# Kernel optimization log

Measured on AMD Instinct MI355X. Metric: run time of the kernel, lower is better.

## Reference

```python
import jax, jax.numpy as jnp
import numpy as np

NUM_COMPONENTS = 8
STRIDE, PADDING, OUTPUT_PADDING, K = 2, 1, 0, 4


def get_comp_mat(n):
    # Cayley-Dickson construction: entry [i, j] = +/- component index of the
    # weight multiplying input component j to produce output component i.
    A = np.array([[0]])
    while A.shape[0] < n:
        m = A.shape[0]
        A = np.vstack([np.hstack([A, -(A + m)]), np.hstack([A + m, A])])
    return A


def setup_inputs() -> dict:
    key = jax.random.key(0)
    k1, k2, k3 = jax.random.split(key, 3)
    B, Cin, Cout, H = 8, 512, 256, 64
    c_in, c_out = Cin // NUM_COMPONENTS, Cout // NUM_COMPONENTS
    x = jax.random.normal(k1, (B, Cin, H, H), jnp.float32)
    # per-component ConvTranspose2d weights, torch layout [C_in, C_out, kH, kW]
    W = jax.random.normal(k2, (NUM_COMPONENTS, c_in, c_out, K, K), jnp.float32) * 0.05
    b = jax.random.normal(k3, (NUM_COMPONENTS, c_out), jnp.float32) * 0.05
    return {"x": x, "W": W, "b": b}


def reference(x, W, b):
    n = NUM_COMPONENTS
    comp = get_comp_mat(n)                 # static [n, n] signed component table
    signs = jnp.asarray(np.where(comp < 0, -1.0, 1.0), x.dtype)
    idx = np.abs(comp)                     # which sub-conv weight to use
    c_in, c_out, kh, kw = W.shape[1:]
    # Fuse the n^2 transpose convs into ONE block transpose conv:
    # Kbig[j*c_in:(j+1)*c_in, i*c_out:(i+1)*c_out] = sign[i,j] * W[idx[i,j]]
    Wsel = W[idx] * signs[:, :, None, None, None, None]          # [ni, nj, c_in, c_out, kh, kw]
    Wbig = jnp.transpose(Wsel, (1, 2, 0, 3, 4, 5)).reshape(n * c_in, n * c_out, kh, kw)
    bbig = jnp.einsum('ij,ijc->ic', signs, b[idx]).reshape(n * c_out)
    # torch ConvTranspose2d == conv with input dilated by stride and flipped kernel
    rhs = jnp.flip(Wbig, (2, 3)).transpose(1, 0, 2, 3)           # OIHW
    pad = K - 1 - PADDING
    out = jax.lax.conv_general_dilated(
        x, rhs, window_strides=(1, 1),
        padding=((pad, pad + OUTPUT_PADDING), (pad, pad + OUTPUT_PADDING)),
        lhs_dilation=(STRIDE, STRIDE),
        dimension_numbers=('NCHW', 'OIHW', 'NCHW'))
    return out + bbig[None, :, None, None]
```

## Files before the change

kernel.cpp:

```cpp
#include <hip/hip_runtime.h>
#include <hip/hip_bf16.h>

typedef unsigned short ushort_t;
typedef __attribute__((ext_vector_type(8))) short short8;
typedef __attribute__((ext_vector_type(4))) float f32x4;

#define NCOMP    8
#define CIN      512
#define COUT     256
#define H        64
#define HP       66
#define OHW      128
#define NB       8

__device__ const int d_idx8[8][8] = {
    {0,1,2,1,4,3,2,3},
    {1,0,3,2,5,4,1,2},
    {2,1,0,1,6,5,4,3},
    {3,2,1,0,7,6,5,4},
    {4,3,2,3,0,1,2,1},
    {5,4,1,2,1,0,3,2},
    {6,5,4,3,2,1,0,1},
    {7,6,5,4,3,2,1,0}};

__device__ const int kh_tab[2][2] = {{1,3},{0,2}};
__device__ const int dh_tab[2][2] = {{0,-1},{1,0}};

__global__ void prep_x2(const float* __restrict__ x, ushort_t* __restrict__ xpadT) {
    __shared__ __align__(16) ushort_t lds[64 * 512];
    const int t = threadIdx.x;
    const int b = blockIdx.y;
    const int ihb = blockIdx.x;

    if (ihb == 64) {
        short8 z = {0,0,0,0,0,0,0,0};
        ushort_t* r0 = xpadT + ((size_t)b * HP + 0)  * HP * CIN;
        ushort_t* r1 = xpadT + ((size_t)b * HP + 65) * HP * CIN;
        for (int e = t; e < (HP * CIN) / 8; e += 256) {
            *(short8*)(r0 + e * 8) = z;
            *(short8*)(r1 + e * 8) = z;
        }
        return;
    }
    const int ih = ihb;

    const int iv      = t & 15;
    const int ic_base = t >> 4;
    const float* xr = x + ((size_t)b * CIN * H + ih) * H;
#pragma unroll 8
    for (int r = 0; r < 32; ++r) {
        const int ic = r * 16 + ic_base;
        const float4 v = *(const float4*)(xr + (size_t)ic * H * H + iv * 4);
        const int swz_ic = ic ^ (iv << 3);
        __hip_bfloat16 h0 = __float2bfloat16(v.x);
        __hip_bfloat16 h1 = __float2bfloat16(v.y);
        __hip_bfloat16 h2 = __float2bfloat16(v.z);
        __hip_bfloat16 h3 = __float2bfloat16(v.w);
        lds[(iv * 4 + 0) * 512 + swz_ic] = *(ushort_t*)&h0;
        lds[(iv * 4 + 1) * 512 + swz_ic] = *(ushort_t*)&h1;
        lds[(iv * 4 + 2) * 512 + swz_ic] = *(ushort_t*)&h2;
        lds[(iv * 4 + 3) * 512 + swz_ic] = *(ushort_t*)&h3;
    }
    __syncthreads();

    ushort_t* rowc = xpadT + (((size_t)b * HP + ih + 1) * HP) * CIN;
    ushort_t* dst  = rowc + CIN;
#pragma unroll
    for (int r = 0; r < 16; ++r) {
        const int e   = r * 256 + t;
        const int iw  = e >> 6;
        const int ic0 = (e & 63) * 8;
        const int off = iw * 512 + (ic0 ^ ((iw >> 2) << 3));
        *(short8*)(dst + (size_t)e * 8) = *(const short8*)(lds + off);
    }
    if (t < 128) {
        short8 z = {0,0,0,0,0,0,0,0};
        const int l = t & 63;
        ushort_t* hc = (t < 64) ? rowc : (rowc + 65 * CIN);
        *(short8*)(hc + l * 8) = z;
    }
}

__global__ void prep_w(const float* __restrict__ W, const float* __restrict__ bias,
                       ushort_t* __restrict__ Abf, float* __restrict__ bbig) {
    const int t = blockIdx.x * blockDim.x + threadIdx.x;
    if (t < 4 * 64 * 256 * 32) {
        int kin = t & 31;
        int oc  = (t >> 5) & 255;
        int ks  = (t >> 13) & 63;
        int cls = t >> 19;
        int k  = ks * 32 + kin;
        int a  = k >> 10, c = (k >> 9) & 1, ic = k & 511;
        int ph = cls >> 1, pw = cls & 1;
        int kh = kh_tab[ph][a], kw = kh_tab[pw][c];
        int i = oc >> 5, co = oc & 31;
        int j = ic >> 6, ci = ic & 63;
        float s = (i >= j) ? 1.0f : -1.0f;
        float v = s * W[(((size_t)(d_idx8[i][j] * 64 + ci) * 32 + co) * 4 + kh) * 4 + kw];
        __hip_bfloat16 h = __float2bfloat16(v);
        Abf[t] = *(ushort_t*)&h;
    }
    if (t < COUT) {
        int i = t >> 5, co = t & 31;
        float acc = 0.0f;
        for (int j = 0; j < NCOMP; ++j)
            acc += ((i >= j) ? 1.0f : -1.0f) * bias[d_idx8[i][j] * 32 + co];
        bbig[t] = acc;
    }
}

__device__ __forceinline__ void async16(void* lds_dst, const void* g_src) {
    __builtin_amdgcn_global_load_lds(
        (const __attribute__((address_space(1))) unsigned int*)g_src,
        (__attribute__((address_space(3))) unsigned int*)lds_dst,
        16, 0, 0);
}

#define STAGE(NS, CB)                                                          \
  {                                                                            \
    const int ns_  = (NS);                                                     \
    const int na_  = ns_ >> 5;                                                 \
    const int ncb_ = (ns_ >> 4) & 1;                                           \
    const int go_  = ((na_ ? dh1 : dh0) * HP + (ncb_ ? dw1 : dw0)) * CIN       \
                     + (ns_ & 15) * 32;                                        \
    const ushort_t* nap_ = Abf_t + (size_t)ns_ * 8192;                         \
    async16(sb + (CB) + t * 16,         nap_);                                 \
    async16(sb + (CB) + 8192 + t * 16,  base_lo + go_);                        \
    async16(sb + (CB) + 16384 + t * 16, base_hi + go_);                        \
  }

#define COMPUTE(CB)                                                            \
  {                                                                            \
    short8 af[4], bf[4];                                                       \
    _Pragma("unroll")                                                          \
    for (int s = 0; s < 4; ++s) {                                              \
      af[s] = *(const short8*)(sb + (CB) + aoff + s * 1024);                   \
      bf[s] = *(const short8*)(sb + (CB) + boff + s * 1024);                   \
    }                                                                          \
    _Pragma("unroll")                                                          \
    for (int sm = 0; sm < 4; ++sm)                                             \
      _Pragma("unroll")                                                        \
      for (int sn = 0; sn < 4; ++sn)                                           \
        acc[sm][sn] = __builtin_amdgcn_mfma_f32_16x16x32_bf16(                 \
            af[sm], bf[sn], acc[sm][sn], 0, 0, 0);                             \
  }

#define WAITBAR(N)                                                             \
  asm volatile("s_waitcnt vmcnt(" #N ")" ::: "memory");                        \
  __builtin_amdgcn_s_barrier();                                                \
  __builtin_amdgcn_sched_barrier(0);

__launch_bounds__(512, 4)
__global__ void htconv_mfma(const ushort_t* __restrict__ xpadT,
                            const ushort_t* __restrict__ Abf,
                            const float* __restrict__ bbig,
                            float* __restrict__ out) {
    __shared__ __align__(16) ushort_t smem[36864];
    char* sb = (char*)smem;

    const int t     = threadIdx.x;
    const int ntile = blockIdx.x;
    const int mtile = blockIdx.y;
    const int cls   = blockIdx.z & 3;
    const int b     = blockIdx.z >> 2;
    const int ph = cls >> 1, pw = cls & 1;
    const int ohh0 = ntile * 4;

    const int srcc = (((t & 3) ^ ((t >> 3) & 3)) * 8);
    const ushort_t* Abf_t =
        Abf + ((size_t)cls * 64) * 8192 + (size_t)mtile * 4096
            + ((size_t)(t >> 2)) * 32 + srcc;

    const int dh0 = dh_tab[ph][0], dh1 = dh_tab[ph][1];
    const int dw0 = dh_tab[pw][0], dw1 = dh_tab[pw][1];
    const int oww = (t >> 2) & 63;
    const int rlo = t >> 8;
    const ushort_t* base_lo =
        xpadT + (((size_t)b * HP + ohh0 + rlo + 1) * HP + oww + 1) * CIN + srcc;
    const ushort_t* base_hi = base_lo + (size_t)2 * HP * CIN;

    const int lane = t & 63, wave = t >> 6;
    const int wm = wave >> 2, wn = wave & 3;
    const int col = lane & 15, quad = lane >> 4;
    const int soff = (quad ^ ((col >> 1) & 3)) * 16;
    const int aoff = (wm * 64 + col) * 64 + soff;
    const int boff = 8192 + (wn * 64 + col) * 64 + soff;

    f32x4 acc[4][4];
#pragma unroll
    for (int i = 0; i < 4; ++i)
#pragma unroll
        for (int j = 0; j < 4; ++j)
            acc[i][j] = (f32x4){0.f, 0.f, 0.f, 0.f};

    STAGE(0, 0);
    STAGE(1, 24576);

#pragma unroll 1
    for (int i = 0; i < 20; ++i) {
        const int n = 3 * i;
        WAITBAR(3); STAGE(n + 2, 49152); COMPUTE(0);
        WAITBAR(3); STAGE(n + 3, 0);     COMPUTE(24576);
        WAITBAR(3); STAGE(n + 4, 24576); COMPUTE(49152);
    }
    WAITBAR(3); STAGE(62, 49152); COMPUTE(0);
    WAITBAR(3); STAGE(63, 0);     COMPUTE(24576);
    WAITBAR(3);                   COMPUTE(49152);
    WAITBAR(0);                   COMPUTE(0);

    const int oh = 2 * (ohh0 + wn) + ph;
#pragma unroll
    for (int sm = 0; sm < 4; ++sm) {
#pragma unroll
        for (int r = 0; r < 4; ++r) {
            const int occ = mtile * 128 + wm * 64 + sm * 16 + quad * 4 + r;
            const float bv = bbig[occ];
            float* obase = out + (((size_t)b * COUT + occ) * OHW + oh) * OHW + pw;
#pragma unroll
            for (int sn = 0; sn < 4; ++sn) {
                const int owi = sn * 16 + col;
                obase[2 * owi] = acc[sm][sn][r] + bv;
            }
        }
    }
}

extern "C" void kernel_launch(void* const* d_in, const int* in_sizes, int n_in,
                              void* d_out, int out_size, void* d_ws, size_t ws_size,
                              hipStream_t stream) {
    const float* x    = (const float*)d_in[0];
    const float* W    = (const float*)d_in[1];
    const float* bias = (const float*)d_in[2];
    float* out = (float*)d_out;

    ushort_t* xpadT = (ushort_t*)d_ws;
    ushort_t* Abf   = xpadT + (size_t)NB * HP * HP * CIN;
    float*    bbig  = (float*)(Abf + (size_t)4 * 64 * 256 * 32);

    prep_x2<<<dim3(65, NB), 256, 0, stream>>>(x, xpadT);
    prep_w<<<dim3((4 * 64 * 256 * 32) / 256), 256, 0, stream>>>(W, bias, Abf, bbig);
    htconv_mfma<<<dim3(16, 2, 32), 512, 0, stream>>>(xpadT, Abf, bbig, out);
}
```

Before: 310.9 us.

## Double-buffer LDS fragment reads in registers to overlap with MFMA

The main loop now software-pipelines the LDS-to-register fragment loads. Each step reads the next stage's A/B fragments into a second register set while issuing MFMAs on the current set, and the loop is unrolled by six to rotate both buffers. The wait before each barrier tightens from vmcnt(3) to vmcnt(0), so each step waits for the async copy issued one step earlier, with less slack for global-load latency. The extra fragment registers may also pressure occupancy under launch_bounds(512,4).

```diff
diff --git a/kernel.cpp b/kernel.cpp
--- a/kernel.cpp
+++ b/kernel.cpp
@@ -129,26 +129,29 @@
     async16(sb + (CB) + 16384 + t * 16, base_hi + go_);                        \
   }
 
-#define COMPUTE(CB)                                                            \
-  {                                                                            \
-    short8 af[4], bf[4];                                                       \
+#define DSREAD(CB, AFS, BFS)                                                   \
     _Pragma("unroll")                                                          \
     for (int s = 0; s < 4; ++s) {                                              \
-      af[s] = *(const short8*)(sb + (CB) + aoff + s * 1024);                   \
-      bf[s] = *(const short8*)(sb + (CB) + boff + s * 1024);                   \
-    }                                                                          \
+      AFS[s] = *(const short8*)(sb + (CB) + aoff + s * 1024);                  \
+      BFS[s] = *(const short8*)(sb + (CB) + boff + s * 1024);                  \
+    }
+
+#define MFMA16(AFS, BFS)                                                       \
     _Pragma("unroll")                                                          \
     for (int sm = 0; sm < 4; ++sm)                                             \
       _Pragma("unroll")                                                        \
       for (int sn = 0; sn < 4; ++sn)                                           \
         acc[sm][sn] = __builtin_amdgcn_mfma_f32_16x16x32_bf16(                 \
-            af[sm], bf[sn], acc[sm][sn], 0, 0, 0);                             \
-  }
-
-#define WAITBAR(N)                                                             \
-  asm volatile("s_waitcnt vmcnt(" #N ")" ::: "memory");                        \
+            AFS[sm], BFS[sn], acc[sm][sn], 0, 0, 0);
+
+#define WB0                                                                    \
+  asm volatile("s_waitcnt vmcnt(0)" ::: "memory");                             \
   __builtin_amdgcn_s_barrier();                                                \
   __builtin_amdgcn_sched_barrier(0);
+
+#define B0 0
+#define B1 24576
+#define B2 49152
 
 __launch_bounds__(512, 4)
 __global__ void htconv_mfma(const ushort_t* __restrict__ xpadT,
@@ -193,20 +196,29 @@
         for (int j = 0; j < 4; ++j)
             acc[i][j] = (f32x4){0.f, 0.f, 0.f, 0.f};
 
-    STAGE(0, 0);
-    STAGE(1, 24576);
+    short8 afA[4], bfA[4], afB[4], bfB[4];
+
+    STAGE(0, B0);
+    STAGE(1, B1);
+    asm volatile("s_waitcnt vmcnt(3)" ::: "memory");
+    __builtin_amdgcn_s_barrier();
+    __builtin_amdgcn_sched_barrier(0);
+    DSREAD(B0, afA, bfA);
 
 #pragma unroll 1
-    for (int i = 0; i < 20; ++i) {
-        const int n = 3 * i;
-        WAITBAR(3); STAGE(n + 2, 49152); COMPUTE(0);
-        WAITBAR(3); STAGE(n + 3, 0);     COMPUTE(24576);
-        WAITBAR(3); STAGE(n + 4, 24576); COMPUTE(49152);
-    }
-    WAITBAR(3); STAGE(62, 49152); COMPUTE(0);
-    WAITBAR(3); STAGE(63, 0);     COMPUTE(24576);
-    WAITBAR(3);                   COMPUTE(49152);
-    WAITBAR(0);                   COMPUTE(0);
+    for (int i = 0; i < 10; ++i) {
+        const int n = 6 * i;
+        WB0; STAGE(n + 2, B2); DSREAD(B1, afB, bfB); MFMA16(afA, bfA);
+        WB0; STAGE(n + 3, B0); DSREAD(B2, afA, bfA); MFMA16(afB, bfB);
+        WB0; STAGE(n + 4, B1); DSREAD(B0, afB, bfB); MFMA16(afA, bfA);
+        WB0; STAGE(n + 5, B2); DSREAD(B1, afA, bfA); MFMA16(afB, bfB);
+        WB0; STAGE(n + 6, B0); DSREAD(B2, afB, bfB); MFMA16(afA, bfA);
+        WB0; STAGE(n + 7, B1); DSREAD(B0, afA, bfA); MFMA16(afB, bfB);
+    }
+    WB0; STAGE(62, B2); DSREAD(B1, afB, bfB); MFMA16(afA, bfA);
+    WB0; STAGE(63, B0); DSREAD(B2, afA, bfA); MFMA16(afB, bfB);
+    WB0;                DSREAD(B0, afB, bfB); MFMA16(afA, bfA);
+    MFMA16(afB, bfB);
 
     const int oh = 2 * (ohh0 + wn) + ph;
 #pragma unroll
```

Result: slower. 355.0 us (+14.2%).

## Load A fragments directly into registers and split prep_x2 by channel halves

Applied to the files above, without the earlier changes.

The main MFMA kernel no longer stages the weight (A) tile through LDS. Each wave loads its A fragments straight from global memory into registers for the next k-step, and only the input (B) tiles stay triple-buffered in LDS. This cuts LDS per block and the associated LDS traffic. The explicit vmcnt waits before barriers are removed, so the correctness of the B buffers now depends on compiler-inserted waits for the register loads. The prep kernel is also split over two channel halves to double its block count and halve its LDS footprint.

```diff
diff --git a/kernel.cpp b/kernel.cpp
--- a/kernel.cpp
+++ b/kernel.cpp
@@ -27,57 +27,55 @@
 __device__ const int dh_tab[2][2] = {{0,-1},{1,0}};
 
 __global__ void prep_x2(const float* __restrict__ x, ushort_t* __restrict__ xpadT) {
-    __shared__ __align__(16) ushort_t lds[64 * 512];
-    const int t = threadIdx.x;
-    const int b = blockIdx.y;
+    __shared__ __align__(16) ushort_t lds[64 * 256];
+    const int t  = threadIdx.x;
+    const int b  = blockIdx.y;
+    const int zh = blockIdx.z;
     const int ihb = blockIdx.x;
 
     if (ihb == 64) {
-        short8 z = {0,0,0,0,0,0,0,0};
-        ushort_t* r0 = xpadT + ((size_t)b * HP + 0)  * HP * CIN;
-        ushort_t* r1 = xpadT + ((size_t)b * HP + 65) * HP * CIN;
-        for (int e = t; e < (HP * CIN) / 8; e += 256) {
-            *(short8*)(r0 + e * 8) = z;
-            *(short8*)(r1 + e * 8) = z;
-        }
+        short8 z8 = {0,0,0,0,0,0,0,0};
+        ushort_t* r0 = xpadT + ((size_t)b * HP + (zh ? 65 : 0)) * HP * CIN;
+        for (int e = t; e < (HP * CIN) / 8; e += 256)
+            *(short8*)(r0 + e * 8) = z8;
         return;
     }
     const int ih = ihb;
 
     const int iv      = t & 15;
     const int ic_base = t >> 4;
-    const float* xr = x + ((size_t)b * CIN * H + ih) * H;
+    const float* xr = x + ((size_t)(b * CIN + zh * 256)) * H * H + (size_t)ih * H;
 #pragma unroll 8
-    for (int r = 0; r < 32; ++r) {
-        const int ic = r * 16 + ic_base;
-        const float4 v = *(const float4*)(xr + (size_t)ic * H * H + iv * 4);
-        const int swz_ic = ic ^ (iv << 3);
+    for (int r = 0; r < 16; ++r) {
+        const int icl = r * 16 + ic_base;
+        const float4 v = *(const float4*)(xr + (size_t)icl * H * H + iv * 4);
+        const int swz = icl ^ (iv << 3);
         __hip_bfloat16 h0 = __float2bfloat16(v.x);
         __hip_bfloat16 h1 = __float2bfloat16(v.y);
         __hip_bfloat16 h2 = __float2bfloat16(v.z);
         __hip_bfloat16 h3 = __float2bfloat16(v.w);
-        lds[(iv * 4 + 0) * 512 + swz_ic] = *(ushort_t*)&h0;
-        lds[(iv * 4 + 1) * 512 + swz_ic] = *(ushort_t*)&h1;
-        lds[(iv * 4 + 2) * 512 + swz_ic] = *(ushort_t*)&h2;
-        lds[(iv * 4 + 3) * 512 + swz_ic] = *(ushort_t*)&h3;
+        lds[(iv * 4 + 0) * 256 + swz] = *(ushort_t*)&h0;
+        lds[(iv * 4 + 1) * 256 + swz] = *(ushort_t*)&h1;
+        lds[(iv * 4 + 2) * 256 + swz] = *(ushort_t*)&h2;
+        lds[(iv * 4 + 3) * 256 + swz] = *(ushort_t*)&h3;
     }
     __syncthreads();
 
     ushort_t* rowc = xpadT + (((size_t)b * HP + ih + 1) * HP) * CIN;
-    ushort_t* dst  = rowc + CIN;
-#pragma unroll
-    for (int r = 0; r < 16; ++r) {
-        const int e   = r * 256 + t;
-        const int iw  = e >> 6;
-        const int ic0 = (e & 63) * 8;
-        const int off = iw * 512 + (ic0 ^ ((iw >> 2) << 3));
-        *(short8*)(dst + (size_t)e * 8) = *(const short8*)(lds + off);
-    }
-    if (t < 128) {
-        short8 z = {0,0,0,0,0,0,0,0};
+    ushort_t* dstb = rowc + CIN + zh * 256;
+#pragma unroll
+    for (int r = 0; r < 8; ++r) {
+        const int e    = r * 256 + t;
+        const int iw   = e >> 5;
+        const int icl0 = (e & 31) * 8;
+        const int off  = iw * 256 + (icl0 ^ ((iw >> 2) << 3));
+        *(short8*)(dstb + (size_t)iw * CIN + icl0) = *(const short8*)(lds + off);
+    }
+    if (zh == 0 && t < 128) {
+        short8 z8 = {0,0,0,0,0,0,0,0};
         const int l = t & 63;
         ushort_t* hc = (t < 64) ? rowc : (rowc + 65 * CIN);
-        *(short8*)(hc + l * 8) = z;
+        *(short8*)(hc + l * 8) = z8;
     }
 }
 
@@ -116,46 +114,67 @@
         16, 0, 0);
 }
 
-#define STAGE(NS, CB)                                                          \
+#define BB0 0
+#define BB1 16384
+#define BB2 32768
+
+#define STAGE_B(NS, CB)                                                        \
   {                                                                            \
     const int ns_  = (NS);                                                     \
     const int na_  = ns_ >> 5;                                                 \
     const int ncb_ = (ns_ >> 4) & 1;                                           \
     const int go_  = ((na_ ? dh1 : dh0) * HP + (ncb_ ? dw1 : dw0)) * CIN       \
                      + (ns_ & 15) * 32;                                        \
-    const ushort_t* nap_ = Abf_t + (size_t)ns_ * 8192;                         \
-    async16(sb + (CB) + t * 16,         nap_);                                 \
-    async16(sb + (CB) + 8192 + t * 16,  base_lo + go_);                        \
-    async16(sb + (CB) + 16384 + t * 16, base_hi + go_);                        \
+    async16(sb + (CB) + t * 16,        base_lo + go_);                         \
+    async16(sb + (CB) + 8192 + t * 16, base_hi + go_);                         \
   }
 
-#define COMPUTE(CB)                                                            \
+#define LOADA(NS)                                                              \
+    _Pragma("unroll")                                                          \
+    for (int s = 0; s < 4; ++s)                                                \
+      af[s] = *(const short8*)(Aptr + (size_t)(NS) * 8192 + s * 512);
+
+#define STEP(NS_ST, CB_ST, CB_RD, NS_A)                                        \
   {                                                                            \
-    short8 af[4], bf[4];                                                       \
-    _Pragma("unroll")                                                          \
-    for (int s = 0; s < 4; ++s) {                                              \
-      af[s] = *(const short8*)(sb + (CB) + aoff + s * 1024);                   \
-      bf[s] = *(const short8*)(sb + (CB) + boff + s * 1024);                   \
-    }                                                                          \
+    __builtin_amdgcn_s_barrier();                                              \
+    __builtin_amdgcn_sched_barrier(0);                                         \
+    STAGE_B(NS_ST, CB_ST);                                                     \
+    short8 bf[4];                                                              \
+    _Pragma("unroll")                                                          \
+    for (int s = 0; s < 4; ++s)                                                \
+      bf[s] = *(const short8*)(sb + (CB_RD) + boff + s * 1024);                \
     _Pragma("unroll")                                                          \
     for (int sm = 0; sm < 4; ++sm)                                             \
       _Pragma("unroll")                                                        \
       for (int sn = 0; sn < 4; ++sn)                                           \
         acc[sm][sn] = __builtin_amdgcn_mfma_f32_16x16x32_bf16(                 \
             af[sm], bf[sn], acc[sm][sn], 0, 0, 0);                             \
+    LOADA(NS_A);                                                               \
   }
 
-#define WAITBAR(N)                                                             \
-  asm volatile("s_waitcnt vmcnt(" #N ")" ::: "memory");                        \
-  __builtin_amdgcn_s_barrier();                                                \
-  __builtin_amdgcn_sched_barrier(0);
+#define STEP_NOST(CB_RD, NS_A)                                                 \
+  {                                                                            \
+    __builtin_amdgcn_s_barrier();                                              \
+    __builtin_amdgcn_sched_barrier(0);                                         \
+    short8 bf[4];                                                              \
+    _Pragma("unroll")                                                          \
+    for (int s = 0; s < 4; ++s)                                                \
+      bf[s] = *(const short8*)(sb + (CB_RD) + boff + s * 1024);                \
+    _Pragma("unroll")                                                          \
+    for (int sm = 0; sm < 4; ++sm)                                             \
+      _Pragma("unroll")                                                        \
+      for (int sn = 0; sn < 4; ++sn)                                           \
+        acc[sm][sn] = __builtin_amdgcn_mfma_f32_16x16x32_bf16(                 \
+            af[sm], bf[sn], acc[sm][sn], 0, 0, 0);                             \
+    LOADA(NS_A);                                                               \
+  }
 
 __launch_bounds__(512, 4)
 __global__ void htconv_mfma(const ushort_t* __restrict__ xpadT,
                             const ushort_t* __restrict__ Abf,
                             const float* __restrict__ bbig,
                             float* __restrict__ out) {
-    __shared__ __align__(16) ushort_t smem[36864];
+    __shared__ __align__(16) ushort_t smem[24576];
     char* sb = (char*)smem;
 
     const int t     = threadIdx.x;
@@ -167,10 +186,6 @@
     const int ohh0 = ntile * 4;
 
     const int srcc = (((t & 3) ^ ((t >> 3) & 3)) * 8);
-    const ushort_t* Abf_t =
-        Abf + ((size_t)cls * 64) * 8192 + (size_t)mtile * 4096
-            + ((size_t)(t >> 2)) * 32 + srcc;
-
     const int dh0 = dh_tab[ph][0], dh1 = dh_tab[ph][1];
     const int dw0 = dh_tab[pw][0], dw1 = dh_tab[pw][1];
     const int oww = (t >> 2) & 63;
@@ -183,8 +198,11 @@
     const int wm = wave >> 2, wn = wave & 3;
     const int col = lane & 15, quad = lane >> 4;
     const int soff = (quad ^ ((col >> 1) & 3)) * 16;
-    const int aoff = (wm * 64 + col) * 64 + soff;
-    const int boff = 8192 + (wn * 64 + col) * 64 + soff;
+    const int boff = (wn * 64 + col) * 64 + soff;
+
+    const ushort_t* Aptr =
+        Abf + (size_t)cls * (64 * 256 * 32)
+            + (size_t)(mtile * 128 + wm * 64 + col) * 32 + quad * 8;
 
     f32x4 acc[4][4];
 #pragma unroll
@@ -193,20 +211,37 @@
         for (int j = 0; j < 4; ++j)
             acc[i][j] = (f32x4){0.f, 0.f, 0.f, 0.f};
 
-    STAGE(0, 0);
-    STAGE(1, 24576);
+    short8 af[4];
+
+    STAGE_B(0, BB0);
+    STAGE_B(1, BB1);
+    LOADA(0);
+    asm volatile("s_waitcnt vmcnt(4)" ::: "memory");
 
 #pragma unroll 1
     for (int i = 0; i < 20; ++i) {
         const int n = 3 * i;
-        WAITBAR(3); STAGE(n + 2, 49152); COMPUTE(0);
-        WAITBAR(3); STAGE(n + 3, 0);     COMPUTE(24576);
-        WAITBAR(3); STAGE(n + 4, 24576); COMPUTE(49152);
-    }
-    WAITBAR(3); STAGE(62, 49152); COMPUTE(0);
-    WAITBAR(3); STAGE(63, 0);     COMPUTE(24576);
-    WAITBAR(3);                   COMPUTE(49152);
-    WAITBAR(0);                   COMPUTE(0);
+        STEP(n + 2, BB2, BB0, n + 1);
+        STEP(n + 3, BB0, BB1, n + 2);
+        STEP(n + 4, BB1, BB2, n + 3);
+    }
+    STEP(62, BB2, BB0, 61);
+    STEP(63, BB0, BB1, 62);
+    STEP_NOST(BB2, 63);
+    {
+        __builtin_amdgcn_s_barrier();
+        __builtin_amdgcn_sched_barrier(0);
+        short8 bf[4];
+#pragma unroll
+        for (int s = 0; s < 4; ++s)
+            bf[s] = *(const short8*)(sb + BB0 + boff + s * 1024);
+#pragma unroll
+        for (int sm = 0; sm < 4; ++sm)
+#pragma unroll
+            for (int sn = 0; sn < 4; ++sn)
+                acc[sm][sn] = __builtin_amdgcn_mfma_f32_16x16x32_bf16(
+                    af[sm], bf[sn], acc[sm][sn], 0, 0, 0);
+    }
 
     const int oh = 2 * (ohh0 + wn) + ph;
 #pragma unroll
@@ -237,7 +272,7 @@
     ushort_t* Abf   = xpadT + (size_t)NB * HP * HP * CIN;
     float*    bbig  = (float*)(Abf + (size_t)4 * 64 * 256 * 32);
 
-    prep_x2<<<dim3(65, NB), 256, 0, stream>>>(x, xpadT);
+    prep_x2<<<dim3(65, NB, 2), 256, 0, stream>>>(x, xpadT);
     prep_w<<<dim3((4 * 64 * 256 * 32) / 256), 256, 0, stream>>>(W, bias, Abf, bbig);
     htconv_mfma<<<dim3(16, 2, 32), 512, 0, stream>>>(xpadT, Abf, bbig, out);
 }
```

Result: slower. 363.2 us (+16.8%).
